# Kernel optimization log

Hardware: AMD Instinct MI355X
Metric: run time of the kernel (lower is better)

Reference implementation:

```python
import jax, jax.numpy as jnp
import numpy as np

H = 50      # hidden_size (fixed in source)
IN = 7      # input_size = len(features)
B = 1024    # batch
T = 512     # seq_len
FC1 = 25
OUT = 1


def setup_inputs() -> dict:
    key = jax.random.key(0)
    ks = jax.random.split(key, 24)
    s = 1.0 / np.sqrt(H)  # PyTorch LSTM/Linear default uniform init scale

    def u(k, shape):
        return jax.random.uniform(k, shape, jnp.float32, -s, s)

    d = {"x": jax.random.normal(ks[0], (B, T, IN), jnp.float32)}
    # 4 stacked LSTM layers total: lstm1 has 2 layers (in=7 then 50), lstm2 has 2 layers (in=50)
    in_sizes = [IN, H, H, H]
    for l, isz in enumerate(in_sizes):
        d[f"Wih{l}"] = u(ks[1 + 4 * l], (4 * H, isz))
        d[f"Whh{l}"] = u(ks[2 + 4 * l], (4 * H, H))
        d[f"bih{l}"] = u(ks[3 + 4 * l], (4 * H,))
        d[f"bhh{l}"] = u(ks[4 + 4 * l], (4 * H,))
    d["W1"] = u(ks[17], (FC1, H))
    d["b1"] = u(ks[18], (FC1,))
    d["W2"] = u(ks[19], (OUT, FC1))
    d["b2"] = u(ks[20], (OUT,))
    return d


def _lstm_layer(x, Wih, Whh, bih, bhh):
    # x: [B, T, in] -> hidden sequence [B, T, H]. PyTorch gate order: i, f, g, o.
    b, t, _ = x.shape
    h = Whh.shape[1]
    # Precompute input projection for all timesteps in one big GEMM: [T, B, 4H]
    xp = jnp.einsum('bti,gi->tbg', x, Wih) + (bih + bhh)

    def step(carry, xt):
        hs, cs = carry
        gates = xt + hs @ Whh.T                      # [B, 4H]
        i, f, g, o = jnp.split(gates, 4, axis=-1)
        i = jax.nn.sigmoid(i)
        f = jax.nn.sigmoid(f)
        g = jnp.tanh(g)
        o = jax.nn.sigmoid(o)
        cs = f * cs + i * g
        hs = o * jnp.tanh(cs)
        return (hs, cs), hs

    h0 = jnp.zeros((b, h), x.dtype)
    _, hseq = jax.lax.scan(step, (h0, h0), xp)       # hseq: [T, B, H]
    return hseq.transpose(1, 0, 2)


def reference(x, Wih0, Whh0, bih0, bhh0, Wih1, Whh1, bih1, bhh1,
              Wih2, Whh2, bih2, bhh2, Wih3, Whh3, bih3, bhh3,
              W1, b1, W2, b2):
    out = x
    layers = [(Wih0, Whh0, bih0, bhh0), (Wih1, Whh1, bih1, bhh1),
              (Wih2, Whh2, bih2, bhh2), (Wih3, Whh3, bih3, bhh3)]
    for Wih, Whh, bih, bhh in layers:
        out = _lstm_layer(out, Wih, Whh, bih, bhh)
    h = out[:, -1, :]                                # last timestep [B, H]
    # dropout is identity in eval mode
    h = jax.nn.relu(h @ W1.T + b1)
    return h @ W2.T + b2                             # [B, 1]
```

## Files before the change

kernel.cpp:

```cpp
#include <hip/hip_runtime.h>


#define H 50
#define INSZ 7
#define BATCH 1024
#define TT 512
#define NL 4
#define FC1N 25
#define BPG 4
#define NBLK (BATCH / BPG)
#define NTHREADS 1024
#define HS 80
#define BIAS0 7
#define BIASL 56

typedef _Float16 half_t;
typedef __attribute__((ext_vector_type(8))) _Float16 half8_t;
typedef __attribute__((ext_vector_type(4))) float float4_t;

struct Params {
  const float* x;
  const float* Wih[NL];
  const float* Whh[NL];
  const float* bih[NL];
  const float* bhh[NL];
  const float* W1;
  const float* b1;
  const float* W2;
  const float* b2;
  float* out;
};

__device__ __forceinline__ float fast_rcp(float x) {
  return __builtin_amdgcn_rcpf(x);
}
__device__ __forceinline__ float fast_exp2(float x) {
  return __builtin_amdgcn_exp2f(x);
}
__device__ __forceinline__ float sigf(float x) {
  return fast_rcp(1.0f + fast_exp2(-1.442695041f * x));
}
__device__ __forceinline__ float tanh_fast(float x) {
  return 2.0f * fast_rcp(1.0f + fast_exp2(-2.885390082f * x)) - 1.0f;
}

__global__ __launch_bounds__(NTHREADS, 4) void lstm_r5(Params p) {
  __shared__ __align__(16) half_t Hbuf[NL][2][BPG][HS];
  __shared__ __align__(16) half_t Xbuf[2][BPG][HS];
  __shared__ float fc_h[BPG][H];
  __shared__ float fc1_buf[BPG][FC1N];

  const int tid = threadIdx.x;
  const int b0 = blockIdx.x * BPG;
  const int lane = tid & 63;
  const int quad = lane >> 4;
  const int col = lane & 15;
  const int glay = tid >> 8;
  const int wl = (((tid >> 6) & 3) + glay) & 3;

  half8_t afrag[4][4];
#pragma unroll
  for (int t4 = 0; t4 < 4; ++t4) {
#pragma unroll
    for (int g = 0; g < 4; ++g) {
      half8_t v;
#pragma unroll
      for (int j = 0; j < 8; ++j) {
        const int r = wl * 64 + t4 * 16 + col;
        const int u = r >> 2, q = r & 3;
        const int k = g * 32 + quad * 8 + j;
        float wv = 0.0f;
        if (u < H) {
          const int row = q * H + u;
          if (glay == 0) {
            if (k < INSZ) wv = p.Wih[0][row * INSZ + k];
            else if (k == BIAS0) wv = p.bih[0][row] + p.bhh[0][row];
            else if (k >= 64 && (k - 64) < H) wv = p.Whh[0][row * H + (k - 64)];
          } else {
            if (k < H) wv = p.Wih[glay][row * H + k];
            else if (k == BIASL) wv = p.bih[glay][row] + p.bhh[glay][row];
            else if (k >= 64 && (k - 64) < H) wv = p.Whh[glay][row * H + (k - 64)];
          }
        }
        v[j] = (half_t)wv;
      }
      afrag[t4][g] = v;
    }
  }

  {
    unsigned* hz = (unsigned*)Hbuf;
    const int nh = NL * 2 * BPG * HS / 2;
    for (int i = tid; i < nh; i += NTHREADS) hz[i] = 0u;
    unsigned* xz = (unsigned*)Xbuf;
    const int nx = 2 * BPG * HS / 2;
    for (int i = tid; i < nx; i += NTHREADS) xz[i] = 0u;
  }
  __syncthreads();
  if (tid < 32) {
    const int l = tid >> 3, pr = (tid >> 2) & 1, b = tid & 3;
    Hbuf[l][pr][b][BIASL] = (half_t)1.0f;
  } else if (tid < 40) {
    const int idx = tid - 32;
    Xbuf[idx >> 2][idx & 3][BIAS0] = (half_t)1.0f;
  }
  if (tid >= 64 && tid < 64 + BPG * INSZ) {
    const int idx = tid - 64, b = idx / INSZ, k = idx % INSZ;
    Xbuf[0][b][k] = (half_t)p.x[((size_t)(b0 + b) * TT + 0) * INSZ + k];
  }
  __syncthreads();

  const int bb = col & 3;
  const int tsel = col >> 2;
  const int uu = 16 * wl + 4 * tsel + quad;
  const bool updact = (uu < H);

  const half_t* inb[2];
  inb[0] = (glay == 0) ? &Xbuf[0][bb][quad * 8] : &Hbuf[glay - 1][1][bb][quad * 8];
  inb[1] = (glay == 0) ? &Xbuf[1][bb][quad * 8] : &Hbuf[glay - 1][0][bb][quad * 8];
  const half_t* ownb[2] = {&Hbuf[glay][0][bb][quad * 8], &Hbuf[glay][1][bb][quad * 8]};
  half_t* stb[2] = {&Hbuf[glay][1][bb][uu], &Hbuf[glay][0][bb][uu]};

  const int xidx = lane - 32;
  const bool xact = (glay == 0) && (wl == 3) && (xidx >= 0) && (xidx < BPG * INSZ);
  const int xb = xact ? xidx / INSZ : 0;
  const int xk = xact ? xidx % INSZ : 0;

  float cst = 0.0f;
  const float4_t fz = {0.0f, 0.0f, 0.0f, 0.0f};

  for (int s = 0; s < TT + NL - 1; ++s) {
    const int t = s - glay;
    const bool act = (t >= 0) && (t < TT);

    float xv = 0.0f;
    if (xact && (s + 1) < TT)
      xv = p.x[((size_t)(b0 + xb) * TT + (s + 1)) * INSZ + xk];

    if (act) {
      const int par = t & 1;
      const half_t* pin = inb[par];
      const half_t* pow_ = ownb[par];
      float4_t a0 = fz, a1 = fz, a2 = fz, a3 = fz;

      if (glay == 0) {
        const half8_t v0 = *(const half8_t*)(pin);
        const half8_t v2 = *(const half8_t*)(pow_);
        const half8_t v3 = *(const half8_t*)(pow_ + 32);
        a0 = __builtin_amdgcn_mfma_f32_16x16x32_f16(afrag[0][0], v0, a0, 0, 0, 0);
        a1 = __builtin_amdgcn_mfma_f32_16x16x32_f16(afrag[1][0], v0, a1, 0, 0, 0);
        a2 = __builtin_amdgcn_mfma_f32_16x16x32_f16(afrag[2][0], v0, a2, 0, 0, 0);
        if (16 * wl < H - 48) {}
        a3 = __builtin_amdgcn_mfma_f32_16x16x32_f16(afrag[3][0], v0, a3, 0, 0, 0);
        a0 = __builtin_amdgcn_mfma_f32_16x16x32_f16(afrag[0][2], v2, a0, 0, 0, 0);
        a1 = __builtin_amdgcn_mfma_f32_16x16x32_f16(afrag[1][2], v2, a1, 0, 0, 0);
        a2 = __builtin_amdgcn_mfma_f32_16x16x32_f16(afrag[2][2], v2, a2, 0, 0, 0);
        a3 = __builtin_amdgcn_mfma_f32_16x16x32_f16(afrag[3][2], v2, a3, 0, 0, 0);
        a0 = __builtin_amdgcn_mfma_f32_16x16x32_f16(afrag[0][3], v3, a0, 0, 0, 0);
        a1 = __builtin_amdgcn_mfma_f32_16x16x32_f16(afrag[1][3], v3, a1, 0, 0, 0);
        a2 = __builtin_amdgcn_mfma_f32_16x16x32_f16(afrag[2][3], v3, a2, 0, 0, 0);
        a3 = __builtin_amdgcn_mfma_f32_16x16x32_f16(afrag[3][3], v3, a3, 0, 0, 0);
      } else {
        const half8_t v0 = *(const half8_t*)(pin);
        const half8_t v1 = *(const half8_t*)(pin + 32);
        const half8_t v2 = *(const half8_t*)(pow_);
        const half8_t v3 = *(const half8_t*)(pow_ + 32);
        if (wl != 3) {
          a0 = __builtin_amdgcn_mfma_f32_16x16x32_f16(afrag[0][0], v0, a0, 0, 0, 0);
          a1 = __builtin_amdgcn_mfma_f32_16x16x32_f16(afrag[1][0], v0, a1, 0, 0, 0);
          a2 = __builtin_amdgcn_mfma_f32_16x16x32_f16(afrag[2][0], v0, a2, 0, 0, 0);
          a3 = __builtin_amdgcn_mfma_f32_16x16x32_f16(afrag[3][0], v0, a3, 0, 0, 0);
          a0 = __builtin_amdgcn_mfma_f32_16x16x32_f16(afrag[0][1], v1, a0, 0, 0, 0);
          a1 = __builtin_amdgcn_mfma_f32_16x16x32_f16(afrag[1][1], v1, a1, 0, 0, 0);
          a2 = __builtin_amdgcn_mfma_f32_16x16x32_f16(afrag[2][1], v1, a2, 0, 0, 0);
          a3 = __builtin_amdgcn_mfma_f32_16x16x32_f16(afrag[3][1], v1, a3, 0, 0, 0);
          a0 = __builtin_amdgcn_mfma_f32_16x16x32_f16(afrag[0][2], v2, a0, 0, 0, 0);
          a1 = __builtin_amdgcn_mfma_f32_16x16x32_f16(afrag[1][2], v2, a1, 0, 0, 0);
          a2 = __builtin_amdgcn_mfma_f32_16x16x32_f16(afrag[2][2], v2, a2, 0, 0, 0);
          a3 = __builtin_amdgcn_mfma_f32_16x16x32_f16(afrag[3][2], v2, a3, 0, 0, 0);
          a0 = __builtin_amdgcn_mfma_f32_16x16x32_f16(afrag[0][3], v3, a0, 0, 0, 0);
          a1 = __builtin_amdgcn_mfma_f32_16x16x32_f16(afrag[1][3], v3, a1, 0, 0, 0);
          a2 = __builtin_amdgcn_mfma_f32_16x16x32_f16(afrag[2][3], v3, a2, 0, 0, 0);
          a3 = __builtin_amdgcn_mfma_f32_16x16x32_f16(afrag[3][3], v3, a3, 0, 0, 0);
        } else {
          a0 = __builtin_amdgcn_mfma_f32_16x16x32_f16(afrag[0][0], v0, a0, 0, 0, 0);
          a0 = __builtin_amdgcn_mfma_f32_16x16x32_f16(afrag[0][1], v1, a0, 0, 0, 0);
          a0 = __builtin_amdgcn_mfma_f32_16x16x32_f16(afrag[0][2], v2, a0, 0, 0, 0);
          a0 = __builtin_amdgcn_mfma_f32_16x16x32_f16(afrag[0][3], v3, a0, 0, 0, 0);
        }
      }

      if (updact) {
        const float4_t g01 = (col & 4) ? a1 : a0;
        const float4_t g23 = (col & 4) ? a3 : a2;
        const float4_t ga = (col & 8) ? g23 : g01;
        const float gi = sigf(ga[0]);
        const float gf = sigf(ga[1]);
        const float gg = tanh_fast(ga[2]);
        const float go = sigf(ga[3]);
        cst = gf * cst + gi * gg;
        const float h = go * tanh_fast(cst);
        *(stb[par]) = (half_t)h;
        if (glay == NL - 1 && t == TT - 1) fc_h[bb][uu] = h;
      }
    }

    if (xact && (s + 1) < TT)
      Xbuf[(s + 1) & 1][xb][xk] = (half_t)xv;
    __syncthreads();
  }

  if (tid < BPG * FC1N) {
    const int b = tid / FC1N, j = tid % FC1N;
    const float* w = p.W1 + j * H;
    float a = p.b1[j];
#pragma unroll
    for (int k = 0; k < H; ++k) a += fc_h[b][k] * w[k];
    fc1_buf[b][j] = fmaxf(a, 0.0f);
  }
  __syncthreads();
  if (tid < BPG) {
    float a = p.b2[0];
#pragma unroll
    for (int j = 0; j < FC1N; ++j) a += fc1_buf[tid][j] * p.W2[j];
    p.out[b0 + tid] = a;
  }
}

extern "C" void kernel_launch(void* const* d_in, const int* in_sizes, int n_in,
                              void* d_out, int out_size, void* d_ws, size_t ws_size,
                              hipStream_t stream) {
  Params p;
  p.x = (const float*)d_in[0];
  for (int l = 0; l < NL; ++l) {
    p.Wih[l] = (const float*)d_in[1 + 4 * l];
    p.Whh[l] = (const float*)d_in[2 + 4 * l];
    p.bih[l] = (const float*)d_in[3 + 4 * l];
    p.bhh[l] = (const float*)d_in[4 + 4 * l];
  }
  p.W1 = (const float*)d_in[17];
  p.b1 = (const float*)d_in[18];
  p.W2 = (const float*)d_in[19];
  p.b2 = (const float*)d_in[20];
  p.out = (float*)d_out;

  hipLaunchKernelGGL(lstm_r5, dim3(NBLK), dim3(NTHREADS), 0, stream, p);
}
```

Before: 574.6 us.

## Stage input sequence in shared ring buffer and unroll time loop by parity

The per-step global load of the next x timestep is replaced by a 64-step shared-memory ring. It is prefilled at start and refilled 32 steps at a time by one wave, which takes the global load latency off the recurrent critical path. The steady-state loop is unrolled by two with parity-resolved buffer pointers, so it no longer checks activity or selects buffers each step. Layer-0 bias moves into the own-hidden slot (k=120), and layer-0's last wave now issues only one MFMA tile. The cost is extra shared memory and a periodic burst of scalar loads inside one step.

```diff
diff --git a/kernel.cpp b/kernel.cpp
--- a/kernel.cpp
+++ b/kernel.cpp
@@ -3,16 +3,16 @@
 
 #define H 50
 #define INSZ 7
-#define BATCH 1024
 #define TT 512
 #define NL 4
 #define FC1N 25
 #define BPG 4
-#define NBLK (BATCH / BPG)
+#define NBLK 256
 #define NTHREADS 1024
 #define HS 80
-#define BIAS0 7
 #define BIASL 56
+#define XRING 64
+#define XB 32
 
 typedef _Float16 half_t;
 typedef __attribute__((ext_vector_type(8))) _Float16 half8_t;
@@ -31,22 +31,18 @@
   float* out;
 };
 
-__device__ __forceinline__ float fast_rcp(float x) {
-  return __builtin_amdgcn_rcpf(x);
-}
-__device__ __forceinline__ float fast_exp2(float x) {
-  return __builtin_amdgcn_exp2f(x);
-}
 __device__ __forceinline__ float sigf(float x) {
-  return fast_rcp(1.0f + fast_exp2(-1.442695041f * x));
+  return __builtin_amdgcn_rcpf(1.0f + __builtin_amdgcn_exp2f(-1.442695041f * x));
 }
 __device__ __forceinline__ float tanh_fast(float x) {
-  return 2.0f * fast_rcp(1.0f + fast_exp2(-2.885390082f * x)) - 1.0f;
-}
-
-__global__ __launch_bounds__(NTHREADS, 4) void lstm_r5(Params p) {
+  return 2.0f * __builtin_amdgcn_rcpf(1.0f + __builtin_amdgcn_exp2f(-2.885390082f * x)) - 1.0f;
+}
+
+#define MFMA16(A, B, C) __builtin_amdgcn_mfma_f32_16x16x32_f16((A), (B), (C), 0, 0, 0)
+
+__global__ __launch_bounds__(NTHREADS, 4) void lstm_r6(Params p) {
   __shared__ __align__(16) half_t Hbuf[NL][2][BPG][HS];
-  __shared__ __align__(16) half_t Xbuf[2][BPG][HS];
+  __shared__ __align__(16) half_t Xstage[XRING][BPG][XB];
   __shared__ float fc_h[BPG][H];
   __shared__ float fc1_buf[BPG][FC1N];
 
@@ -74,8 +70,8 @@
           const int row = q * H + u;
           if (glay == 0) {
             if (k < INSZ) wv = p.Wih[0][row * INSZ + k];
-            else if (k == BIAS0) wv = p.bih[0][row] + p.bhh[0][row];
             else if (k >= 64 && (k - 64) < H) wv = p.Whh[0][row * H + (k - 64)];
+            else if (k == 120) wv = p.bih[0][row] + p.bhh[0][row];
           } else {
             if (k < H) wv = p.Wih[glay][row * H + k];
             else if (k == BIASL) wv = p.bih[glay][row] + p.bhh[glay][row];
@@ -92,21 +88,19 @@
     unsigned* hz = (unsigned*)Hbuf;
     const int nh = NL * 2 * BPG * HS / 2;
     for (int i = tid; i < nh; i += NTHREADS) hz[i] = 0u;
-    unsigned* xz = (unsigned*)Xbuf;
-    const int nx = 2 * BPG * HS / 2;
+    unsigned* xz = (unsigned*)Xstage;
+    const int nx = XRING * BPG * XB / 2;
     for (int i = tid; i < nx; i += NTHREADS) xz[i] = 0u;
   }
   __syncthreads();
   if (tid < 32) {
     const int l = tid >> 3, pr = (tid >> 2) & 1, b = tid & 3;
     Hbuf[l][pr][b][BIASL] = (half_t)1.0f;
-  } else if (tid < 40) {
-    const int idx = tid - 32;
-    Xbuf[idx >> 2][idx & 3][BIAS0] = (half_t)1.0f;
-  }
-  if (tid >= 64 && tid < 64 + BPG * INSZ) {
-    const int idx = tid - 64, b = idx / INSZ, k = idx % INSZ;
-    Xbuf[0][b][k] = (half_t)p.x[((size_t)(b0 + b) * TT + 0) * INSZ + k];
+  }
+  for (int i = tid; i < XRING * BPG * INSZ; i += NTHREADS) {
+    const int t = i / (BPG * INSZ), rem = i % (BPG * INSZ);
+    const int b = rem / INSZ, k = rem % INSZ;
+    Xstage[t][b][k] = (half_t)p.x[((size_t)(b0 + b) * TT + t) * INSZ + k];
   }
   __syncthreads();
 
@@ -116,97 +110,128 @@
   const bool updact = (uu < H);
 
   const half_t* inb[2];
-  inb[0] = (glay == 0) ? &Xbuf[0][bb][quad * 8] : &Hbuf[glay - 1][1][bb][quad * 8];
-  inb[1] = (glay == 0) ? &Xbuf[1][bb][quad * 8] : &Hbuf[glay - 1][0][bb][quad * 8];
+  inb[0] = (glay == 0) ? (const half_t*)Xstage : &Hbuf[glay - 1][1][bb][quad * 8];
+  inb[1] = (glay == 0) ? (const half_t*)Xstage : &Hbuf[glay - 1][0][bb][quad * 8];
   const half_t* ownb[2] = {&Hbuf[glay][0][bb][quad * 8], &Hbuf[glay][1][bb][quad * 8]};
   half_t* stb[2] = {&Hbuf[glay][1][bb][uu], &Hbuf[glay][0][bb][uu]};
 
-  const int xidx = lane - 32;
-  const bool xact = (glay == 0) && (wl == 3) && (xidx >= 0) && (xidx < BPG * INSZ);
-  const int xb = xact ? xidx / INSZ : 0;
-  const int xk = xact ? xidx % INSZ : 0;
+  const int pe = glay & 1, po = pe ^ 1;
+  const half_t* in_e = inb[pe];
+  const half_t* in_o = inb[po];
+  const half_t* own_e = ownb[pe];
+  const half_t* own_o = ownb[po];
+  half_t* st_e = stb[pe];
+  half_t* st_o = stb[po];
+  const half_t* xrb = &Xstage[0][bb][quad * 8];
+
+  const bool xwave = (glay == 0) && (wl == 3);
+  const int rb = lane >> 5;
+  const int rt = lane & 31;
 
   float cst = 0.0f;
-  const float4_t fz = {0.0f, 0.0f, 0.0f, 0.0f};
-
-  for (int s = 0; s < TT + NL - 1; ++s) {
+
+#define TICK_BODY(PIN, POWN, PST, FCW)                                          \
+  {                                                                             \
+    const float4_t fz_ = {0.0f, 0.0f, 0.0f, 0.0f};                              \
+    float4_t a0 = fz_, a1 = fz_, a2 = fz_, a3 = fz_;                            \
+    if (glay == 0) {                                                            \
+      const half8_t v0 = *(const half8_t*)(PIN);                                \
+      const half8_t v2 = *(const half8_t*)(POWN);                               \
+      const half8_t v3 = *(const half8_t*)((POWN) + 32);                        \
+      if (wl != 3) {                                                            \
+        a0 = MFMA16(afrag[0][0], v0, a0); a1 = MFMA16(afrag[1][0], v0, a1);     \
+        a2 = MFMA16(afrag[2][0], v0, a2); a3 = MFMA16(afrag[3][0], v0, a3);     \
+        a0 = MFMA16(afrag[0][2], v2, a0); a1 = MFMA16(afrag[1][2], v2, a1);     \
+        a2 = MFMA16(afrag[2][2], v2, a2); a3 = MFMA16(afrag[3][2], v2, a3);     \
+        a0 = MFMA16(afrag[0][3], v3, a0); a1 = MFMA16(afrag[1][3], v3, a1);     \
+        a2 = MFMA16(afrag[2][3], v3, a2); a3 = MFMA16(afrag[3][3], v3, a3);     \
+      } else {                                                                  \
+        a0 = MFMA16(afrag[0][0], v0, a0);                                       \
+        a0 = MFMA16(afrag[0][2], v2, a0);                                       \
+        a0 = MFMA16(afrag[0][3], v3, a0);                                       \
+      }                                                                         \
+    } else {                                                                    \
+      const half8_t v0 = *(const half8_t*)(PIN);                                \
+      const half8_t v1 = *(const half8_t*)((PIN) + 32);                         \
+      const half8_t v2 = *(const half8_t*)(POWN);                               \
+      const half8_t v3 = *(const half8_t*)((POWN) + 32);                        \
+      if (wl != 3) {                                                            \
+        a0 = MFMA16(afrag[0][0], v0, a0); a1 = MFMA16(afrag[1][0], v0, a1);     \
+        a2 = MFMA16(afrag[2][0], v0, a2); a3 = MFMA16(afrag[3][0], v0, a3);     \
+        a0 = MFMA16(afrag[0][1], v1, a0); a1 = MFMA16(afrag[1][1], v1, a1);     \
+        a2 = MFMA16(afrag[2][1], v1, a2); a3 = MFMA16(afrag[3][1], v1, a3);     \
+        a0 = MFMA16(afrag[0][2], v2, a0); a1 = MFMA16(afrag[1][2], v2, a1);     \
+        a2 = MFMA16(afrag[2][2], v2, a2); a3 = MFMA16(afrag[3][2], v2, a3);     \
+        a0 = MFMA16(afrag[0][3], v3, a0); a1 = MFMA16(afrag[1][3], v3, a1);     \
+        a2 = MFMA16(afrag[2][3], v3, a2); a3 = MFMA16(afrag[3][3], v3, a3);     \
+      } else {                                                                  \
+        a0 = MFMA16(afrag[0][0], v0, a0);                                       \
+        a0 = MFMA16(afrag[0][1], v1, a0);                                       \
+        a0 = MFMA16(afrag[0][2], v2, a0);                                       \
+        a0 = MFMA16(afrag[0][3], v3, a0);                                       \
+      }                                                                         \
+    }                                                                           \
+    if (updact) {                                                               \
+      const float4_t g01 = (col & 4) ? a1 : a0;                                 \
+      const float4_t g23 = (col & 4) ? a3 : a2;                                 \
+      const float4_t ga = (col & 8) ? g23 : g01;                                \
+      const float gi = sigf(ga[0]);                                             \
+      const float gf = sigf(ga[1]);                                             \
+      const float gg = tanh_fast(ga[2]);                                        \
+      const float go = sigf(ga[3]);                                             \
+      cst = gf * cst + gi * gg;                                                 \
+      const float h = go * tanh_fast(cst);                                      \
+      *(PST) = (half_t)h;                                                       \
+      if (FCW) fc_h[bb][uu] = h;                                                \
+    }                                                                           \
+  }
+
+  for (int s = 0; s < 3; ++s) {
     const int t = s - glay;
-    const bool act = (t >= 0) && (t < TT);
-
-    float xv = 0.0f;
-    if (xact && (s + 1) < TT)
-      xv = p.x[((size_t)(b0 + xb) * TT + (s + 1)) * INSZ + xk];
-
-    if (act) {
+    if (t >= 0) {
       const int par = t & 1;
-      const half_t* pin = inb[par];
-      const half_t* pow_ = ownb[par];
-      float4_t a0 = fz, a1 = fz, a2 = fz, a3 = fz;
-
-      if (glay == 0) {
-        const half8_t v0 = *(const half8_t*)(pin);
-        const half8_t v2 = *(const half8_t*)(pow_);
-        const half8_t v3 = *(const half8_t*)(pow_ + 32);
-        a0 = __builtin_amdgcn_mfma_f32_16x16x32_f16(afrag[0][0], v0, a0, 0, 0, 0);
-        a1 = __builtin_amdgcn_mfma_f32_16x16x32_f16(afrag[1][0], v0, a1, 0, 0, 0);
-        a2 = __builtin_amdgcn_mfma_f32_16x16x32_f16(afrag[2][0], v0, a2, 0, 0, 0);
-        if (16 * wl < H - 48) {}
-        a3 = __builtin_amdgcn_mfma_f32_16x16x32_f16(afrag[3][0], v0, a3, 0, 0, 0);
-        a0 = __builtin_amdgcn_mfma_f32_16x16x32_f16(afrag[0][2], v2, a0, 0, 0, 0);
-        a1 = __builtin_amdgcn_mfma_f32_16x16x32_f16(afrag[1][2], v2, a1, 0, 0, 0);
-        a2 = __builtin_amdgcn_mfma_f32_16x16x32_f16(afrag[2][2], v2, a2, 0, 0, 0);
-        a3 = __builtin_amdgcn_mfma_f32_16x16x32_f16(afrag[3][2], v2, a3, 0, 0, 0);
-        a0 = __builtin_amdgcn_mfma_f32_16x16x32_f16(afrag[0][3], v3, a0, 0, 0, 0);
-        a1 = __builtin_amdgcn_mfma_f32_16x16x32_f16(afrag[1][3], v3, a1, 0, 0, 0);
-        a2 = __builtin_amdgcn_mfma_f32_16x16x32_f16(afrag[2][3], v3, a2, 0, 0, 0);
-        a3 = __builtin_amdgcn_mfma_f32_16x16x32_f16(afrag[3][3], v3, a3, 0, 0, 0);
-      } else {
-        const half8_t v0 = *(const half8_t*)(pin);
-        const half8_t v1 = *(const half8_t*)(pin + 32);
-        const half8_t v2 = *(const half8_t*)(pow_);
-        const half8_t v3 = *(const half8_t*)(pow_ + 32);
-        if (wl != 3) {
-          a0 = __builtin_amdgcn_mfma_f32_16x16x32_f16(afrag[0][0], v0, a0, 0, 0, 0);
-          a1 = __builtin_amdgcn_mfma_f32_16x16x32_f16(afrag[1][0], v0, a1, 0, 0, 0);
-          a2 = __builtin_amdgcn_mfma_f32_16x16x32_f16(afrag[2][0], v0, a2, 0, 0, 0);
-          a3 = __builtin_amdgcn_mfma_f32_16x16x32_f16(afrag[3][0], v0, a3, 0, 0, 0);
-          a0 = __builtin_amdgcn_mfma_f32_16x16x32_f16(afrag[0][1], v1, a0, 0, 0, 0);
-          a1 = __builtin_amdgcn_mfma_f32_16x16x32_f16(afrag[1][1], v1, a1, 0, 0, 0);
-          a2 = __builtin_amdgcn_mfma_f32_16x16x32_f16(afrag[2][1], v1, a2, 0, 0, 0);
-          a3 = __builtin_amdgcn_mfma_f32_16x16x32_f16(afrag[3][1], v1, a3, 0, 0, 0);
-          a0 = __builtin_amdgcn_mfma_f32_16x16x32_f16(afrag[0][2], v2, a0, 0, 0, 0);
-          a1 = __builtin_amdgcn_mfma_f32_16x16x32_f16(afrag[1][2], v2, a1, 0, 0, 0);
-          a2 = __builtin_amdgcn_mfma_f32_16x16x32_f16(afrag[2][2], v2, a2, 0, 0, 0);
-          a3 = __builtin_amdgcn_mfma_f32_16x16x32_f16(afrag[3][2], v2, a3, 0, 0, 0);
-          a0 = __builtin_amdgcn_mfma_f32_16x16x32_f16(afrag[0][3], v3, a0, 0, 0, 0);
-          a1 = __builtin_amdgcn_mfma_f32_16x16x32_f16(afrag[1][3], v3, a1, 0, 0, 0);
-          a2 = __builtin_amdgcn_mfma_f32_16x16x32_f16(afrag[2][3], v3, a2, 0, 0, 0);
-          a3 = __builtin_amdgcn_mfma_f32_16x16x32_f16(afrag[3][3], v3, a3, 0, 0, 0);
-        } else {
-          a0 = __builtin_amdgcn_mfma_f32_16x16x32_f16(afrag[0][0], v0, a0, 0, 0, 0);
-          a0 = __builtin_amdgcn_mfma_f32_16x16x32_f16(afrag[0][1], v1, a0, 0, 0, 0);
-          a0 = __builtin_amdgcn_mfma_f32_16x16x32_f16(afrag[0][2], v2, a0, 0, 0, 0);
-          a0 = __builtin_amdgcn_mfma_f32_16x16x32_f16(afrag[0][3], v3, a0, 0, 0, 0);
+      const half_t* pin = (glay == 0) ? (xrb + (t & 63) * (BPG * XB)) : inb[par];
+      TICK_BODY(pin, ownb[par], stb[par], false)
+    }
+    __syncthreads();
+  }
+
+  for (int s = 3; s < 511; s += 2) {
+    {
+      const int t = s - glay;
+      const half_t* pin = (glay == 0) ? (xrb + (s & 63) * (BPG * XB)) : in_o;
+      TICK_BODY(pin, own_o, st_o, false)
+    }
+    __syncthreads();
+    {
+      const int s2 = s + 1;
+      if (xwave && (s2 & 31) == 8 && s2 < 480) {
+        const int tb = (s2 & ~31) + 32;
+#pragma unroll
+        for (int pp = 0; pp < 2; ++pp) {
+          const int b = rb + 2 * pp;
+          const int t = tb + rt;
+          const float* src = &p.x[((size_t)(b0 + b) * TT + t) * INSZ];
+          half_t* dst = &Xstage[t & 63][b][0];
+#pragma unroll
+          for (int k = 0; k < INSZ; ++k) dst[k] = (half_t)src[k];
         }
       }
-
-      if (updact) {
-        const float4_t g01 = (col & 4) ? a1 : a0;
-        const float4_t g23 = (col & 4) ? a3 : a2;
-        const float4_t ga = (col & 8) ? g23 : g01;
-        const float gi = sigf(ga[0]);
-        const float gf = sigf(ga[1]);
-        const float gg = tanh_fast(ga[2]);
-        const float go = sigf(ga[3]);
-        cst = gf * cst + gi * gg;
-        const float h = go * tanh_fast(cst);
-        *(stb[par]) = (half_t)h;
-        if (glay == NL - 1 && t == TT - 1) fc_h[bb][uu] = h;
-      }
-    }
-
-    if (xact && (s + 1) < TT)
-      Xbuf[(s + 1) & 1][xb][xk] = (half_t)xv;
+      const int t = s2 - glay;
+      const half_t* pin = (glay == 0) ? (xrb + (s2 & 63) * (BPG * XB)) : in_e;
+      TICK_BODY(pin, own_e, st_e, false)
+    }
+    __syncthreads();
+  }
+
+  for (int s = 511; s < TT + NL - 1; ++s) {
+    const int t = s - glay;
+    if (t < TT) {
+      const int par = t & 1;
+      const half_t* pin = (glay == 0) ? (xrb + (t & 63) * (BPG * XB)) : inb[par];
+      const bool fcw = (glay == NL - 1) && (t == TT - 1);
+      TICK_BODY(pin, ownb[par], stb[par], fcw)
+    }
     __syncthreads();
   }
 
@@ -244,5 +269,5 @@
   p.b2 = (const float*)d_in[20];
   p.out = (float*)d_out;
 
-  hipLaunchKernelGGL(lstm_r5, dim3(NBLK), dim3(NTHREADS), 0, stream, p);
-}
+  hipLaunchKernelGGL(lstm_r6, dim3(NBLK), dim3(NTHREADS), 0, stream, p);
+}
```

Result: faster. 489.7 us (-14.8%).
